# Optimization experiments

Measured on AMD Instinct MI355X. Metric: run time of the kernel, lower is better.

## Reference

```python
import jax, jax.numpy as jnp
import numpy as np

B, S, DM = 2, 2048, 1024
H, KH, HD = 16, 4, 64  # query heads, kv heads, head_dim
N_REP = H // KH


def rotate_half(u):
    d = u.shape[-1] // 2
    return jnp.concatenate([-u[..., d:], u[..., :d]], axis=-1)


def setup_inputs() -> dict:
    key = jax.random.key(0)
    ks = jax.random.split(key, 7)
    x = jax.random.normal(ks[0], (B, S, DM), dtype=jnp.float32)
    # RoPE tables (real rotary angles for realism)
    inv_freq = 1.0 / (10000.0 ** (jnp.arange(0, HD, 2, dtype=jnp.float32) / HD))
    t = jnp.arange(S, dtype=jnp.float32)
    freqs = jnp.outer(t, inv_freq)                      # [S, HD/2]
    emb = jnp.concatenate([freqs, freqs], axis=-1)      # [S, HD]
    cos, sin = jnp.cos(emb), jnp.sin(emb)
    sc = 0.02
    wq = jax.random.normal(ks[1], (DM, H * HD), dtype=jnp.float32) * sc
    wk = jax.random.normal(ks[2], (DM, KH * HD), dtype=jnp.float32) * sc
    wv = jax.random.normal(ks[3], (DM, KH * HD), dtype=jnp.float32) * sc
    wo = jax.random.normal(ks[4], (H * HD, DM), dtype=jnp.float32) * sc
    return {"x": x, "cos": cos, "sin": sin, "wq": wq, "wk": wk, "wv": wv, "wo": wo}


def reference(x, cos, sin, wq, wk, wv, wo):
    b, s, _ = x.shape
    # QKV projections (no bias)
    q = (x @ wq).reshape(b, s, H, HD)   # [b,s,H,HD]
    k = (x @ wk).reshape(b, s, KH, HD)  # [b,s,KH,HD]
    v = (x @ wv).reshape(b, s, KH, HD)
    # RoPE, broadcast cos/sin over the head axis
    c = cos[None, :s, None, :]
    sn = sin[None, :s, None, :]
    q = q * c + rotate_half(q) * sn
    k = k * c + rotate_half(k) * sn
    # GQA: repeat kv heads (repeat_interleave along head axis)
    k = jnp.repeat(k, N_REP, axis=2)  # [b,s,H,HD]
    v = jnp.repeat(v, N_REP, axis=2)
    # causal attention, full score matrix (non-flash path)
    scores = jnp.einsum("bqhd,bkhd->bhqk", q, k) / jnp.sqrt(jnp.float32(HD))
    causal = jnp.tril(jnp.ones((s, s), dtype=bool))
    scores = jnp.where(causal[None, None], scores, jnp.float32(-jnp.inf))
    attn = jax.nn.softmax(scores, axis=-1)
    out = jnp.einsum("bhqk,bkhd->bqhd", attn, v).reshape(b, s, H * HD)
    return out @ wo
```

## Files before the change

### kernel.cpp

```cpp
#include <hip/hip_runtime.h>
#include <hip/hip_bf16.h>

#define BATCH 2
#define SLEN  2048
#define DM    1024
#define NH    16
#define NKH   4
#define HD    64

typedef __attribute__((ext_vector_type(8))) short short8;
typedef __attribute__((ext_vector_type(4))) float f32x4;

static __device__ __forceinline__ short f2bf(float x) {
    unsigned u = __float_as_uint(x);
    u += 0x7fffu + ((u >> 16) & 1u);
    return (short)(u >> 16);
}

static __device__ __forceinline__ void ldg_lds16(const short* g, short* l) {
    __builtin_amdgcn_global_load_lds(
        (const __attribute__((address_space(1))) unsigned int*)(const void*)g,
        (__attribute__((address_space(3))) unsigned int*)(void*)l,
        16, 0, 0);
}

#define QSCALE 0.1803368801f

__global__ void cvt_bf16(const float* __restrict__ X, short* __restrict__ Xb, int total8)
{
    const int i = blockIdx.x * blockDim.x + threadIdx.x;
    if (i >= total8) return;
    const float4 v0 = ((const float4*)X)[i * 2];
    const float4 v1 = ((const float4*)X)[i * 2 + 1];
    __align__(16) short o[8];
    o[0] = f2bf(v0.x); o[1] = f2bf(v0.y); o[2] = f2bf(v0.z); o[3] = f2bf(v0.w);
    o[4] = f2bf(v1.x); o[5] = f2bf(v1.y); o[6] = f2bf(v1.z); o[7] = f2bf(v1.w);
    ((int4*)Xb)[i] = *(const int4*)o;
}

__global__ __launch_bounds__(256) void wtrans_all(
    const float* __restrict__ wq, const float* __restrict__ wk,
    const float* __restrict__ wv, const float* __restrict__ wo,
    short* __restrict__ T)
{
    const int by = blockIdx.y;
    const float* W; int Nc, rowoff, ntile;
    if (by < 16)      { W = wq; Nc = 1024; rowoff = 0;    ntile = by; }
    else if (by < 20) { W = wk; Nc = 256;  rowoff = 1024; ntile = by - 16; }
    else if (by < 24) { W = wv; Nc = 256;  rowoff = 1280; ntile = by - 20; }
    else              { W = wo; Nc = 1024; rowoff = 1536; ntile = by - 24; }
    const int kt = blockIdx.x * 64;
    const int nt = ntile * 64;
    const int t  = threadIdx.x;
    __shared__ float tile[64][65];

#pragma unroll
    for (int i = 0; i < 4; ++i) {
        const int r = (t >> 4) + i * 16;
        const int c = (t & 15) * 4;
        const float4 v = *(const float4*)(W + (size_t)(kt + r) * Nc + nt + c);
        tile[r][c + 0] = v.x; tile[r][c + 1] = v.y;
        tile[r][c + 2] = v.z; tile[r][c + 3] = v.w;
    }
    __syncthreads();
#pragma unroll
    for (int i = 0; i < 2; ++i) {
        const int rr = (t >> 3) + i * 32;
        const int cc = (t & 7) * 8;
        __align__(16) short o[8];
#pragma unroll
        for (int j = 0; j < 8; ++j) o[j] = f2bf(tile[cc + j][rr]);
        *(int4*)(T + (size_t)(rowoff + nt + rr) * 1024 + kt + cc) = *(const int4*)o;
    }
}

template<int MODE>
__global__ __launch_bounds__(256) void gemm_abt(
    const short* __restrict__ A, const short* __restrict__ Bt,
    int M, int N, int K,
    float* __restrict__ Cf,
    short* __restrict__ Qb, short* __restrict__ Kb, short* __restrict__ Vt,
    const float* __restrict__ cosp, const float* __restrict__ sinp)
{
    const int t    = threadIdx.x;
    const int lane = t & 63;
    const int w    = t >> 6;
    const int l15  = lane & 15;
    const int l4   = lane >> 4;
    const int n0   = blockIdx.x * 128;
    const int m0   = blockIdx.y * 128;
    const int wm   = (w & 1) * 64;
    const int wn   = (w >> 1) * 64;

    __shared__ __align__(16) short As[128 * 32];
    __shared__ __align__(16) short Bs[128 * 32];

    f32x4 acc[4][4];
#pragma unroll
    for (int i = 0; i < 4; ++i)
#pragma unroll
        for (int j = 0; j < 4; ++j) acc[i][j] = (f32x4){0.f, 0.f, 0.f, 0.f};

    for (int kt = 0; kt < K; kt += 32) {
        __syncthreads();
#pragma unroll
        for (int i = 0; i < 2; ++i) {
            const int chunk = i * 256 + t;
            const int r = chunk >> 2;
            const int c = (chunk & 3) * 8;
            ldg_lds16(A  + (size_t)(m0 + r) * K + kt + c, &As[chunk * 8]);
            ldg_lds16(Bt + (size_t)(n0 + r) * K + kt + c, &Bs[chunk * 8]);
        }
        __syncthreads();

        short8 af[4], bf[4];
#pragma unroll
        for (int i = 0; i < 4; ++i)
            af[i] = *(const short8*)&As[(wm + i * 16 + l15) * 32 + l4 * 8];
#pragma unroll
        for (int j = 0; j < 4; ++j)
            bf[j] = *(const short8*)&Bs[(wn + j * 16 + l15) * 32 + l4 * 8];
#pragma unroll
        for (int i = 0; i < 4; ++i)
#pragma unroll
            for (int j = 0; j < 4; ++j)
                acc[i][j] = __builtin_amdgcn_mfma_f32_16x16x32_bf16(af[i], bf[j], acc[i][j], 0, 0, 0);
    }

    if (MODE == 1) {
#pragma unroll
        for (int i = 0; i < 4; ++i)
#pragma unroll
            for (int j = 0; j < 4; ++j)
#pragma unroll
                for (int r = 0; r < 4; ++r) {
                    const int m = m0 + wm + i * 16 + l4 * 4 + r;
                    const int n = n0 + wn + j * 16 + l15;
                    Cf[(size_t)m * N + n] = acc[i][j][r];
                }
        return;
    }

    const int colbase = n0 + wn;
    if (colbase < 1024) {
        const int h = colbase >> 6;
#pragma unroll
        for (int i = 0; i < 4; ++i)
#pragma unroll
            for (int r = 0; r < 4; ++r) {
                const int m = m0 + wm + i * 16 + l4 * 4 + r;
                const int b = m >> 11, s = m & (SLEN - 1);
                short* dst = Qb + (((size_t)(b * SLEN + s) * NH + h) << 6);
#pragma unroll
                for (int j = 0; j < 2; ++j) {
                    const int d = j * 16 + l15;
                    const float cv = cosp[s * HD + d];
                    const float sv = sinp[s * HD + d];
                    const float a0 = acc[i][j][r];
                    const float a1 = acc[i][j + 2][r];
                    dst[d]      = f2bf((a0 * cv - a1 * sv) * QSCALE);
                    dst[d + 32] = f2bf((a1 * cv + a0 * sv) * QSCALE);
                }
            }
    } else if (colbase < 1280) {
        const int kh = (colbase - 1024) >> 6;
#pragma unroll
        for (int i = 0; i < 4; ++i)
#pragma unroll
            for (int r = 0; r < 4; ++r) {
                const int m = m0 + wm + i * 16 + l4 * 4 + r;
                const int b = m >> 11, s = m & (SLEN - 1);
                short* dst = Kb + (((size_t)(b * SLEN + s) * NKH + kh) << 6);
#pragma unroll
                for (int j = 0; j < 2; ++j) {
                    const int d = j * 16 + l15;
                    const float cv = cosp[s * HD + d];
                    const float sv = sinp[s * HD + d];
                    const float a0 = acc[i][j][r];
                    const float a1 = acc[i][j + 2][r];
                    dst[d]      = f2bf(a0 * cv - a1 * sv);
                    dst[d + 32] = f2bf(a1 * cv + a0 * sv);
                }
            }
    } else {
        const int kh = (colbase - 1280) >> 6;
#pragma unroll
        for (int i = 0; i < 4; ++i)
#pragma unroll
            for (int r = 0; r < 4; ++r) {
                const int m = m0 + wm + i * 16 + l4 * 4 + r;
                const int b = m >> 11, s = m & (SLEN - 1);
                const int sp = (s & ~63) | ((s & 15) << 2) | ((s & 63) >> 4);
#pragma unroll
                for (int j = 0; j < 4; ++j) {
                    const int d = j * 16 + l15;
                    Vt[((size_t)((b * NKH + kh) * HD + d)) * SLEN + sp] = f2bf(acc[i][j][r]);
                }
            }
    }
}

#define KVSTR 72

__global__ __launch_bounds__(256, 4) void flash_mfma(
    const short* __restrict__ Qb,
    const short* __restrict__ Kb,
    const short* __restrict__ Vt,
    short* __restrict__ O)
{
    const int qs   = gridDim.x - 1 - blockIdx.x;
    const int kh   = blockIdx.y;
    const int b    = blockIdx.z;
    const int t    = threadIdx.x;
    const int lane = t & 63;
    const int w    = t >> 6;
    const int h    = kh * 4 + w;
    const int l15  = lane & 15;
    const int l4   = lane >> 4;
    const int q0   = qs * 32;

    __shared__ __align__(16) short Ks[64 * KVSTR];
    __shared__ __align__(16) short Vs[64 * KVSTR];
    __shared__ __align__(16) short Ps[4][32 * KVSTR];

    short8 aq[2][2];
#pragma unroll
    for (int i = 0; i < 2; ++i)
#pragma unroll
        for (int ks = 0; ks < 2; ++ks)
            aq[i][ks] = *(const short8*)(
                Qb + ((size_t)((b * SLEN + q0 + i * 16 + l15) * NH + h)) * HD + ks * 32 + l4 * 8);

    f32x4 acc[2][4];
    f32x4 accl[2];
#pragma unroll
    for (int i = 0; i < 2; ++i) {
#pragma unroll
        for (int nt = 0; nt < 4; ++nt) acc[i][nt] = (f32x4){0.f, 0.f, 0.f, 0.f};
        accl[i] = (f32x4){0.f, 0.f, 0.f, 0.f};
    }

    const short8 ones8 = {0x3f80, 0x3f80, 0x3f80, 0x3f80, 0x3f80, 0x3f80, 0x3f80, 0x3f80};

    const int iters = (q0 >> 6) + 1;
    for (int kt = 0; kt < iters; ++kt) {
        const int k0 = kt * 64;
        __syncthreads();
#pragma unroll
        for (int i = 0; i < 2; ++i) {
            const int chunk = i * 256 + t;
            const int r = chunk >> 3;
            const int c = (chunk & 7) * 8;
            *(int4*)&Ks[r * KVSTR + c] =
                *(const int4*)(Kb + ((size_t)((b * SLEN + k0 + r) * NKH + kh)) * HD + c);
            *(int4*)&Vs[r * KVSTR + c] =
                *(const int4*)(Vt + ((size_t)((b * NKH + kh) * HD + r)) * SLEN + k0 + c);
        }
        __syncthreads();

        f32x4 sf[2][4];
#pragma unroll
        for (int i = 0; i < 2; ++i)
#pragma unroll
            for (int f = 0; f < 4; ++f) sf[i][f] = (f32x4){0.f, 0.f, 0.f, 0.f};
#pragma unroll
        for (int ks = 0; ks < 2; ++ks)
#pragma unroll
            for (int f = 0; f < 4; ++f) {
                const short8 bk = *(const short8*)&Ks[(f * 16 + l15) * KVSTR + ks * 32 + l4 * 8];
#pragma unroll
                for (int i = 0; i < 2; ++i)
                    sf[i][f] = __builtin_amdgcn_mfma_f32_16x16x32_bf16(aq[i][ks], bk, sf[i][f], 0, 0, 0);
            }

        if (kt == iters - 1) {
#pragma unroll
            for (int i = 0; i < 2; ++i)
#pragma unroll
                for (int f = 0; f < 4; ++f)
#pragma unroll
                    for (int r = 0; r < 4; ++r)
                        if (k0 + f * 16 + l15 > q0 + i * 16 + l4 * 4 + r)
                            sf[i][f][r] = -1e30f;
        }

#pragma unroll
        for (int i = 0; i < 2; ++i)
#pragma unroll
            for (int r = 0; r < 4; ++r) {
                __align__(8) short pk[4];
#pragma unroll
                for (int f = 0; f < 4; ++f) pk[f] = f2bf(exp2f(sf[i][f][r]));
                *(int2*)&Ps[w][(i * 16 + l4 * 4 + r) * KVSTR + 4 * l15] = *(const int2*)pk;
            }

#pragma unroll
        for (int ks = 0; ks < 2; ++ks) {
            short8 ap[2];
#pragma unroll
            for (int i = 0; i < 2; ++i)
                ap[i] = *(const short8*)&Ps[w][(i * 16 + l15) * KVSTR + ks * 32 + l4 * 8];
#pragma unroll
            for (int nt = 0; nt < 4; ++nt) {
                const short8 bv = *(const short8*)&Vs[(nt * 16 + l15) * KVSTR + ks * 32 + l4 * 8];
#pragma unroll
                for (int i = 0; i < 2; ++i)
                    acc[i][nt] = __builtin_amdgcn_mfma_f32_16x16x32_bf16(ap[i], bv, acc[i][nt], 0, 0, 0);
            }
#pragma unroll
            for (int i = 0; i < 2; ++i)
                accl[i] = __builtin_amdgcn_mfma_f32_16x16x32_bf16(ap[i], ones8, accl[i], 0, 0, 0);
        }
    }

#pragma unroll
    for (int i = 0; i < 2; ++i) {
        float rl[4];
#pragma unroll
        for (int r = 0; r < 4; ++r) rl[r] = 1.f / accl[i][r];
#pragma unroll
        for (int nt = 0; nt < 4; ++nt)
#pragma unroll
            for (int r = 0; r < 4; ++r) {
                const int q = q0 + i * 16 + l4 * 4 + r;
                O[((size_t)((b * SLEN + q) * NH + h)) * HD + nt * 16 + l15] =
                    f2bf(acc[i][nt][r] * rl[r]);
            }
    }
}

extern "C" void kernel_launch(void* const* d_in, const int* in_sizes, int n_in,
                              void* d_out, int out_size, void* d_ws, size_t ws_size,
                              hipStream_t stream) {
    const float* x    = (const float*)d_in[0];
    const float* cosp = (const float*)d_in[1];
    const float* sinp = (const float*)d_in[2];
    const float* wq   = (const float*)d_in[3];
    const float* wk   = (const float*)d_in[4];
    const float* wv   = (const float*)d_in[5];
    const float* wo   = (const float*)d_in[6];
    float* out = (float*)d_out;

    const int Mrows = BATCH * SLEN;

    short* xb = (short*)d_ws;
    short* Ob = xb;
    short* wT = xb + (size_t)Mrows * 1024;
    short* Qb = wT + (size_t)2560 * 1024;
    short* Kb = Qb + (size_t)Mrows * 1024;
    short* Vt = Kb + (size_t)Mrows * 256;

    cvt_bf16<<<(Mrows * DM / 8 + 255) / 256, 256, 0, stream>>>(x, xb, Mrows * DM / 8);

    wtrans_all<<<dim3(16, 40), 256, 0, stream>>>(wq, wk, wv, wo, wT);

    gemm_abt<0><<<dim3(1536 / 128, Mrows / 128), 256, 0, stream>>>(
        xb, wT, Mrows, 1536, DM, nullptr, Qb, Kb, Vt, cosp, sinp);

    flash_mfma<<<dim3(SLEN / 32, NKH, BATCH), 256, 0, stream>>>(Qb, Kb, Vt, Ob);

    gemm_abt<1><<<dim3(DM / 128, Mrows / 128), 256, 0, stream>>>(
        Ob, wT + (size_t)1536 * 1024, Mrows, DM, DM, out,
        nullptr, nullptr, nullptr, nullptr, nullptr);
}
```

Before: 229.8 us.

## Split causal attention over key chunks with partial-sum combine and separate V transpose

The flash attention kernel is split across up to four key chunks of 512 positions each, so long query rows run in parallel blocks rather than one long serial loop. Each chunk writes unnormalized fp32 partial outputs and row sums, which a new combine kernel adds and normalizes. Because the softmax skips max subtraction, the partials can simply be summed. The V projection now writes row-major, and a separate transpose kernel builds the permuted Vt layout instead of scattered strided stores from the GEMM epilogue. This evens out load across the causal triangle, at the cost of two extra launches and extra fp32 partial traffic.

Result: faster. 204.2 us (-11.1%).

```diff
diff --git a/kernel.cpp b/kernel.cpp
--- a/kernel.cpp
+++ b/kernel.cpp
@@ -7,6 +7,9 @@
 #define NH    16
 #define NKH   4
 #define HD    64
+#define NCH   4
+#define PSTRIDE (BATCH * SLEN * NH * HD)
+#define LSTRIDE (BATCH * SLEN * NH)
 
 typedef __attribute__((ext_vector_type(8))) short short8;
 typedef __attribute__((ext_vector_type(4))) float f32x4;
@@ -79,7 +82,7 @@
     const short* __restrict__ A, const short* __restrict__ Bt,
     int M, int N, int K,
     float* __restrict__ Cf,
-    short* __restrict__ Qb, short* __restrict__ Kb, short* __restrict__ Vt,
+    short* __restrict__ Qb, short* __restrict__ Kb, short* __restrict__ Vb,
     const float* __restrict__ cosp, const float* __restrict__ sinp)
 {
     const int t    = threadIdx.x;
@@ -190,13 +193,45 @@
             for (int r = 0; r < 4; ++r) {
                 const int m = m0 + wm + i * 16 + l4 * 4 + r;
                 const int b = m >> 11, s = m & (SLEN - 1);
-                const int sp = (s & ~63) | ((s & 15) << 2) | ((s & 63) >> 4);
-#pragma unroll
-                for (int j = 0; j < 4; ++j) {
-                    const int d = j * 16 + l15;
-                    Vt[((size_t)((b * NKH + kh) * HD + d)) * SLEN + sp] = f2bf(acc[i][j][r]);
-                }
-            }
+                short* dst = Vb + (((size_t)(b * SLEN + s) * NKH + kh) << 6);
+#pragma unroll
+                for (int j = 0; j < 4; ++j)
+                    dst[j * 16 + l15] = f2bf(acc[i][j][r]);
+            }
+    }
+}
+
+__global__ __launch_bounds__(256) void vtrans_b(
+    const short* __restrict__ Vb, short* __restrict__ Vt)
+{
+    const int s0 = blockIdx.x * 64;
+    const int kh = blockIdx.y;
+    const int b  = blockIdx.z;
+    const int t  = threadIdx.x;
+    __shared__ short tile[64][72];
+
+#pragma unroll
+    for (int i = 0; i < 2; ++i) {
+        const int chunk = i * 256 + t;
+        const int r = chunk >> 3;
+        const int c = (chunk & 7) * 8;
+        *(int4*)&tile[r][c] =
+            *(const int4*)(Vb + (((size_t)(b * SLEN + s0 + r) * NKH + kh) << 6) + c);
+    }
+    __syncthreads();
+#pragma unroll
+    for (int i = 0; i < 2; ++i) {
+        const int chunk = i * 256 + t;
+        const int d  = chunk >> 3;
+        const int sc = (chunk & 7) * 8;
+        __align__(16) short o[8];
+#pragma unroll
+        for (int j = 0; j < 8; ++j) {
+            const int sp = sc + j;
+            const int u  = ((sp & 3) << 4) | (sp >> 2);
+            o[j] = tile[u][d];
+        }
+        *(int4*)(Vt + ((size_t)((b * NKH + kh) * HD + d)) * SLEN + s0 + sc) = *(const int4*)o;
     }
 }
 
@@ -206,11 +241,15 @@
     const short* __restrict__ Qb,
     const short* __restrict__ Kb,
     const short* __restrict__ Vt,
-    short* __restrict__ O)
-{
-    const int qs   = gridDim.x - 1 - blockIdx.x;
-    const int kh   = blockIdx.y;
-    const int b    = blockIdx.z;
+    short* __restrict__ O,
+    float* __restrict__ Op,
+    float* __restrict__ Lp)
+{
+    const int qs = 63 - blockIdx.x;
+    const int kc = blockIdx.y & 3;
+    if (kc * 16 > qs) return;
+    const int kh = blockIdx.y >> 2;
+    const int b  = blockIdx.z;
     const int t    = threadIdx.x;
     const int lane = t & 63;
     const int w    = t >> 6;
@@ -242,8 +281,11 @@
 
     const short8 ones8 = {0x3f80, 0x3f80, 0x3f80, 0x3f80, 0x3f80, 0x3f80, 0x3f80, 0x3f80};
 
-    const int iters = (q0 >> 6) + 1;
-    for (int kt = 0; kt < iters; ++kt) {
+    const int ntiles = (q0 >> 6) + 1;
+    const int kt0  = kc * 8;
+    const int kend = (kt0 + 8 < ntiles) ? kt0 + 8 : ntiles;
+
+    for (int kt = kt0; kt < kend; ++kt) {
         const int k0 = kt * 64;
         __syncthreads();
 #pragma unroll
@@ -273,7 +315,7 @@
                     sf[i][f] = __builtin_amdgcn_mfma_f32_16x16x32_bf16(aq[i][ks], bk, sf[i][f], 0, 0, 0);
             }
 
-        if (kt == iters - 1) {
+        if (kt == ntiles - 1) {
 #pragma unroll
             for (int i = 0; i < 2; ++i)
 #pragma unroll
@@ -313,20 +355,69 @@
         }
     }
 
-#pragma unroll
-    for (int i = 0; i < 2; ++i) {
-        float rl[4];
-#pragma unroll
-        for (int r = 0; r < 4; ++r) rl[r] = 1.f / accl[i][r];
-#pragma unroll
-        for (int nt = 0; nt < 4; ++nt)
-#pragma unroll
-            for (int r = 0; r < 4; ++r) {
-                const int q = q0 + i * 16 + l4 * 4 + r;
-                O[((size_t)((b * SLEN + q) * NH + h)) * HD + nt * 16 + l15] =
-                    f2bf(acc[i][nt][r] * rl[r]);
-            }
-    }
+    if (q0 < 512) {
+#pragma unroll
+        for (int i = 0; i < 2; ++i) {
+            float rl[4];
+#pragma unroll
+            for (int r = 0; r < 4; ++r) rl[r] = 1.f / accl[i][r];
+#pragma unroll
+            for (int nt = 0; nt < 4; ++nt)
+#pragma unroll
+                for (int r = 0; r < 4; ++r) {
+                    const int q = q0 + i * 16 + l4 * 4 + r;
+                    O[((size_t)((b * SLEN + q) * NH + h)) * HD + nt * 16 + l15] =
+                        f2bf(acc[i][nt][r] * rl[r]);
+                }
+        }
+    } else {
+        const size_t pbase = (size_t)kc * PSTRIDE;
+#pragma unroll
+        for (int i = 0; i < 2; ++i)
+#pragma unroll
+            for (int nt = 0; nt < 4; ++nt)
+#pragma unroll
+                for (int r = 0; r < 4; ++r) {
+                    const int q = q0 + i * 16 + l4 * 4 + r;
+                    Op[pbase + ((size_t)((b * SLEN + q) * NH + h)) * HD + nt * 16 + l15] =
+                        acc[i][nt][r];
+                }
+        if (l15 == 0) {
+#pragma unroll
+            for (int i = 0; i < 2; ++i)
+#pragma unroll
+                for (int r = 0; r < 4; ++r) {
+                    const int q = q0 + i * 16 + l4 * 4 + r;
+                    Lp[(size_t)kc * LSTRIDE + (size_t)(b * SLEN + q) * NH + h] = accl[i][r];
+                }
+        }
+    }
+}
+
+__global__ void combine_k(const float* __restrict__ Op, const float* __restrict__ Lp,
+                          short* __restrict__ O)
+{
+    const int idx = blockIdx.x * 256 + threadIdx.x;
+    const int dq = idx & 15;
+    const int h  = (idx >> 4) & 15;
+    const int rr = idx >> 8;
+    const int b  = rr / 1536;
+    const int s  = 512 + (rr - b * 1536);
+    const int nact = (s >> 9) + 1;
+    const size_t row = (size_t)(b * SLEN + s) * NH + h;
+
+    float4 o = {0.f, 0.f, 0.f, 0.f};
+    float l = 0.f;
+    for (int kc = 0; kc < nact; ++kc) {
+        const float4 p = *(const float4*)(Op + (size_t)kc * PSTRIDE + row * HD + dq * 4);
+        o.x += p.x; o.y += p.y; o.z += p.z; o.w += p.w;
+        l += Lp[(size_t)kc * LSTRIDE + row];
+    }
+    const float rl = 1.f / l;
+    __align__(8) short pk[4];
+    pk[0] = f2bf(o.x * rl); pk[1] = f2bf(o.y * rl);
+    pk[2] = f2bf(o.z * rl); pk[3] = f2bf(o.w * rl);
+    *(int2*)(O + row * HD + dq * 4) = *(const int2*)pk;
 }
 
 extern "C" void kernel_launch(void* const* d_in, const int* in_sizes, int n_in,
@@ -349,15 +440,23 @@
     short* Qb = wT + (size_t)2560 * 1024;
     short* Kb = Qb + (size_t)Mrows * 1024;
     short* Vt = Kb + (size_t)Mrows * 256;
+    short* Vb = Vt + (size_t)Mrows * 256;
+    float* Op = (float*)(Vb + (size_t)Mrows * 256);
+    float* Lp = Op + (size_t)NCH * PSTRIDE;
 
     cvt_bf16<<<(Mrows * DM / 8 + 255) / 256, 256, 0, stream>>>(x, xb, Mrows * DM / 8);
 
     wtrans_all<<<dim3(16, 40), 256, 0, stream>>>(wq, wk, wv, wo, wT);
 
     gemm_abt<0><<<dim3(1536 / 128, Mrows / 128), 256, 0, stream>>>(
-        xb, wT, Mrows, 1536, DM, nullptr, Qb, Kb, Vt, cosp, sinp);
-
-    flash_mfma<<<dim3(SLEN / 32, NKH, BATCH), 256, 0, stream>>>(Qb, Kb, Vt, Ob);
+        xb, wT, Mrows, 1536, DM, nullptr, Qb, Kb, Vb, cosp, sinp);
+
+    vtrans_b<<<dim3(SLEN / 64, NKH, BATCH), 256, 0, stream>>>(Vb, Vt);
+
+    flash_mfma<<<dim3(SLEN / 32, NKH * NCH, BATCH), 256, 0, stream>>>(
+        Qb, Kb, Vt, Ob, Op, Lp);
+
+    combine_k<<<(BATCH * 1536 * NH * 16) / 256, 256, 0, stream>>>(Op, Lp, Ob);
 
     gemm_abt<1><<<dim3(DM / 128, Mrows / 128), 256, 0, stream>>>(
         Ob, wT + (size_t)1536 * 1024, Mrows, DM, DM, out,
```
